# Performance work log

Hardware: AMD Instinct MI355X
Metric: run time of the kernel (lower is better)

The kernel has to match this reference:

```python
import math
import jax, jax.numpy as jnp
import numpy as np

B, N, D_FULL, M, D_V = 8, 4096, 256, 256, 256


def _phi(x, omega):
    # x: [..., N, d_full], omega: [M, d_full] -> [..., N, M]
    proj = x @ omega.T
    log_phi = proj - 0.5 * jnp.sum(x * x, axis=-1, keepdims=True)
    log_phi = log_phi - jnp.max(log_phi, axis=-1, keepdims=True)
    return jnp.exp(log_phi) / math.sqrt(omega.shape[0])


def _causal(phi_q, phi_k, V):
    # phi_q/phi_k: [B, N, M], V: [B, N, d_v]
    b, n, m = phi_q.shape
    d_v = V.shape[-1]

    def step(carry, inp):
        S, z = carry
        pq, pk, v = inp  # [B,M], [B,M], [B,d_v]
        S = S + pk[:, :, None] * v[:, None, :]          # [B, M, d_v]
        z = z + pk                                       # [B, M]
        num = jnp.einsum('bi,bij->bj', pq, S)            # [B, d_v]
        den = jnp.maximum(jnp.sum(pq * z, axis=-1), 1e-6)
        return (S, z), num / den[:, None]

    S0 = jnp.zeros((b, m, d_v), phi_q.dtype)
    z0 = jnp.zeros((b, m), phi_q.dtype)
    xs = (jnp.swapaxes(phi_q, 0, 1), jnp.swapaxes(phi_k, 0, 1), jnp.swapaxes(V, 0, 1))
    _, ys = jax.lax.scan(step, (S0, z0), xs)  # ys: [N, B, d_v]
    return jnp.swapaxes(ys, 0, 1)


def setup_inputs() -> dict:
    key = jax.random.key(0)
    kq, kk, kv, ko = jax.random.split(key, 4)
    Q = jax.random.normal(kq, (B, N, D_FULL), dtype=jnp.float32)
    K_in = jax.random.normal(kk, (B, N, D_FULL), dtype=jnp.float32)
    V = jax.random.normal(kv, (B, N, D_V), dtype=jnp.float32)
    omega = jax.random.normal(ko, (M, D_FULL), dtype=jnp.float32)
    return {"Q": Q, "K_in": K_in, "V": V, "omega": omega, "causal": 1}


def reference(Q, K_in, V, omega, causal):
    phi_q = _phi(Q, omega)
    phi_k = _phi(K_in, omega)
    if causal:
        return _causal(phi_q, phi_k, V)
    S = jnp.einsum('bni,bnj->bij', phi_k, V)          # [B, M, d_v]
    z = jnp.sum(phi_k, axis=-2)                        # [B, M]
    num = jnp.einsum('bni,bij->bnj', phi_q, S)
    den = jnp.maximum(jnp.einsum('bni,bi->bn', phi_q, z), 1e-6)
    return num / den[..., None]
```

## Files before the change

### kernel.cpp

```cpp
#include <hip/hip_runtime.h>

#define BN 8
#define NN 4096
#define DD 256
#define MM 256
#define DV 256
#define CHUNK 256
#define NC (NN / CHUNK)

using f32x4 = __attribute__((ext_vector_type(4))) float;
using s16x8 = __attribute__((ext_vector_type(8))) short;

#define MFMA16(a, b, c) __builtin_amdgcn_mfma_f32_16x16x32_bf16(a, b, c, 0, 0, 0)

__device__ __forceinline__ unsigned short f2bf(float x) {
    union { float f; unsigned int u; } v; v.f = x;
    unsigned int r = v.u + 0x7FFF + ((v.u >> 16) & 1);
    return (unsigned short)(r >> 16);
}
__device__ __forceinline__ float bf2f(unsigned short u) {
    union { unsigned int u; float f; } v; v.u = ((unsigned int)u) << 16;
    return v.f;
}

__device__ __forceinline__ void split8(const float4 xa, const float4 xb,
                                       s16x8& ah, s16x8& al)
{
    const float xs[8] = {xa.x, xa.y, xa.z, xa.w, xb.x, xb.y, xb.z, xb.w};
#pragma unroll
    for (int j = 0; j < 8; ++j) {
        union { float f; unsigned u; } v; v.f = xs[j];
        const unsigned hm = v.u & 0xFFFF0000u;
        union { unsigned u; float f; } hv; hv.u = hm;
        ah[j] = (short)(hm >> 16);
        al[j] = (short)f2bf(xs[j] - hv.f);
    }
}

__global__ __launch_bounds__(256) void omconv(
    const float* __restrict__ Om, unsigned short* __restrict__ OmH,
    unsigned short* __restrict__ OmL)
{
    const int i = blockIdx.x * 256 + threadIdx.x;
    const float4 v = *(const float4*)(Om + (size_t)i * 4);
    const float xs[4] = {v.x, v.y, v.z, v.w};
    unsigned short h[4], l[4];
#pragma unroll
    for (int j = 0; j < 4; ++j) {
        h[j] = f2bf(xs[j]);
        l[j] = f2bf(xs[j] - bf2f(h[j]));
    }
    *(uint2*)(OmH + (size_t)i * 4) = *(uint2*)h;
    *(uint2*)(OmL + (size_t)i * 4) = *(uint2*)l;
}

__global__ __launch_bounds__(256, 4) void phi_fused(
    const float* __restrict__ Qp, const float* __restrict__ Kp,
    const unsigned short* __restrict__ OmH, const unsigned short* __restrict__ OmL,
    unsigned short* __restrict__ PhiQ, unsigned short* __restrict__ PhiK,
    unsigned short* __restrict__ PhiT, float* __restrict__ Zp)
{
    const int tid = threadIdx.x;
    const int w = tid >> 6;
    const int lane = tid & 63;
    const int col = lane & 15, quad = lane >> 4;
    const bool kpath = blockIdx.x < 1024;
    const int id = kpath ? blockIdx.x : (blockIdx.x - 1024);
    const float* __restrict__ X = kpath ? Kp : Qp;
    unsigned short* __restrict__ Phi = kpath ? PhiK : PhiQ;
    const long r0 = (long)id * 32;

    __shared__ __align__(16) short AhS[32][264];
    __shared__ __align__(16) short AlS[32][264];
    __shared__ float rowmax_s[32];
    float (*red)[68] = (float(*)[68])AhS;
    unsigned short (*P)[264] = (unsigned short(*)[264])AlS;
    unsigned int* P32 = (unsigned int*)AlS;

    {
        const int rsub = lane >> 5;
        const int cc = lane & 31;
        float4 va[4], vb[4];
#pragma unroll
        for (int j = 0; j < 4; ++j) {
            const int row = w * 8 + j * 2 + rsub;
            const float* p = X + (r0 + row) * DD + cc * 8;
            va[j] = *(const float4*)p;
            vb[j] = *(const float4*)(p + 4);
        }
#pragma unroll
        for (int j = 0; j < 4; ++j) {
            const int row = w * 8 + j * 2 + rsub;
            s16x8 ah, al;
            split8(va[j], vb[j], ah, al);
            *(s16x8*)&AhS[row][cc * 8] = ah;
            *(s16x8*)&AlS[row][cc * 8] = al;
        }
    }

    f32x4 acc[2][4] = {};
    s16x8 bh0[4], bl0[4], bh1[4], bl1[4];
#pragma unroll
    for (int ct = 0; ct < 4; ++ct) {
        const size_t off = (size_t)(w * 64 + ct * 16 + col) * DD + quad * 8;
        bh0[ct] = *(const s16x8*)(OmH + off);
        bl0[ct] = *(const s16x8*)(OmL + off);
    }
    __syncthreads();

#pragma unroll
    for (int kt = 0; kt < 8; ++kt) {
        if (kt < 7) {
#pragma unroll
            for (int ct = 0; ct < 4; ++ct) {
                const size_t off = (size_t)(w * 64 + ct * 16 + col) * DD + (kt + 1) * 32 + quad * 8;
                bh1[ct] = *(const s16x8*)(OmH + off);
                bl1[ct] = *(const s16x8*)(OmL + off);
            }
        }
#pragma unroll
        for (int t = 0; t < 2; ++t) {
            const s16x8 ah = *(const s16x8*)&AhS[t * 16 + col][kt * 32 + quad * 8];
            const s16x8 al = *(const s16x8*)&AlS[t * 16 + col][kt * 32 + quad * 8];
#pragma unroll
            for (int ct = 0; ct < 4; ++ct) {
                acc[t][ct] = MFMA16(ah, bh0[ct], acc[t][ct]);
                acc[t][ct] = MFMA16(ah, bl0[ct], acc[t][ct]);
                acc[t][ct] = MFMA16(al, bh0[ct], acc[t][ct]);
            }
        }
#pragma unroll
        for (int ct = 0; ct < 4; ++ct) { bh0[ct] = bh1[ct]; bl0[ct] = bl1[ct]; }
    }

    __syncthreads();
#pragma unroll
    for (int t = 0; t < 2; ++t)
#pragma unroll
        for (int r = 0; r < 4; ++r) {
            float m = acc[t][0][r];
#pragma unroll
            for (int ct = 1; ct < 4; ++ct) m = fmaxf(m, acc[t][ct][r]);
            red[t * 16 + quad * 4 + r][w * 16 + col] = m;
        }
    __syncthreads();
    {
        const int row = tid >> 3, seg = tid & 7;
        float m = red[row][seg * 8];
#pragma unroll
        for (int j = 1; j < 8; ++j) m = fmaxf(m, red[row][seg * 8 + j]);
        m = fmaxf(m, __shfl_xor(m, 1));
        m = fmaxf(m, __shfl_xor(m, 2));
        m = fmaxf(m, __shfl_xor(m, 4));
        if (seg == 0) rowmax_s[row] = m;
    }
    __syncthreads();

#pragma unroll
    for (int t = 0; t < 2; ++t)
#pragma unroll
        for (int r = 0; r < 4; ++r) {
            const int n = t * 16 + quad * 4 + r;
            const float rm = rowmax_s[n];
#pragma unroll
            for (int ct = 0; ct < 4; ++ct) {
                const float val = __expf(acc[t][ct][r] - rm) * 0.0625f;
                const unsigned u = (unsigned)f2bf(val);
                const unsigned up = (unsigned)__shfl_xor((int)u, 1);
                if ((col & 1) == 0)
                    P32[n * 132 + w * 32 + ct * 8 + (col >> 1)] = u | (up << 16);
            }
        }
    __syncthreads();

    {
        const int t7 = tid & 7;
        const int nb = tid >> 3;
#pragma unroll
        for (int s = 0; s < 4; ++s)
            *(uint4*)(Phi + (r0 + nb) * MM + t7 * 8 + s * 64) =
                *(const uint4*)&P[nb][t7 * 8 + s * 64];
    }

    if (kpath) {
        const int b = id >> 7;
        const int c = (id >> 3) & 15;
        const int n0 = (id & 127) * 32;
        const int m0 = tid & 31;
        const int nsub = tid >> 5;
#pragma unroll
        for (int mi = 0; mi < 8; ++mi) {
            const int m = mi * 32 + m0;
            unsigned short u[4];
#pragma unroll
            for (int j = 0; j < 4; ++j) u[j] = P[nsub * 4 + j][m];
            *(uint2*)(PhiT + ((size_t)b * MM + m) * NN + n0 + nsub * 4) = *(uint2*)u;
        }
        float z = 0.f;
#pragma unroll
        for (int n = 0; n < 32; ++n) z += bf2f(P[n][tid]);
        atomicAdd(&Zp[((b * NC + c) << 8) + tid], z);
    }
}

__global__ __launch_bounds__(256) void transpose_v(
    const float* __restrict__ V, unsigned short* __restrict__ VT)
{
    const int tid = threadIdx.x;
    const int ct = blockIdx.x & 3;
    const long r0 = (long)(blockIdx.x >> 2) * 64;
    const int b = (int)(r0 >> 12);
    const int n0 = (int)(r0 & (NN - 1));
    __shared__ unsigned short T[64][72];
    const int rr = tid >> 4, cs = tid & 15;
#pragma unroll
    for (int p = 0; p < 4; ++p) {
        const int r = p * 16 + rr;
        const float4 v = *(const float4*)(V + (r0 + r) * DV + ct * 64 + cs * 4);
        T[cs * 4 + 0][r] = f2bf(v.x); T[cs * 4 + 1][r] = f2bf(v.y);
        T[cs * 4 + 2][r] = f2bf(v.z); T[cs * 4 + 3][r] = f2bf(v.w);
    }
    __syncthreads();
    const int cl = tid >> 3, ns = tid & 7;
#pragma unroll
    for (int p = 0; p < 2; ++p) {
        const int c = p * 32 + cl;
        *(uint4*)(VT + ((size_t)b * DV + ct * 64 + c) * NN + n0 + ns * 8) = *(uint4*)&T[c][ns * 8];
    }
}

__global__ __launch_bounds__(256, 3) void state_mfma(
    const unsigned short* __restrict__ VT, const unsigned short* __restrict__ PkT,
    unsigned short* __restrict__ ST)
{
    const int tid = threadIdx.x;
    const int w = tid >> 6;
    const int lane = tid & 63;
    const int col = lane & 15, quad = lane >> 4;
    const int q  = blockIdx.x >> 7;
    const int bc = blockIdx.x & 127;
    const int c  = bc & 15;
    const int b  = bc >> 4;
    const int dv0 = (q & 1) * 128 + (w & 1) * 64;
    const int m0  = (q >> 1) * 128 + (w >> 1) * 64;
    const unsigned short* Ab = VT  + (size_t)b * DV * NN + (size_t)c * CHUNK;
    const unsigned short* Bb = PkT + (size_t)b * MM * NN + (size_t)c * CHUNK;

    f32x4 acc[4][4] = {};
    s16x8 a0[4], b0[4], a1[4], b1[4];
#pragma unroll
    for (int t = 0; t < 4; ++t) {
        a0[t] = *(const s16x8*)(Ab + (size_t)(dv0 + t * 16 + col) * NN + quad * 8);
        b0[t] = *(const s16x8*)(Bb + (size_t)(m0 + t * 16 + col) * NN + quad * 8);
    }
#pragma unroll
    for (int kt = 0; kt < 8; ++kt) {
        if (kt < 7) {
#pragma unroll
            for (int t = 0; t < 4; ++t) {
                a1[t] = *(const s16x8*)(Ab + (size_t)(dv0 + t * 16 + col) * NN + (kt + 1) * 32 + quad * 8);
                b1[t] = *(const s16x8*)(Bb + (size_t)(m0 + t * 16 + col) * NN + (kt + 1) * 32 + quad * 8);
            }
        }
#pragma unroll
        for (int i = 0; i < 4; ++i)
#pragma unroll
            for (int j = 0; j < 4; ++j) acc[i][j] = MFMA16(a0[i], b0[j], acc[i][j]);
#pragma unroll
        for (int t = 0; t < 4; ++t) { a0[t] = a1[t]; b0[t] = b1[t]; }
    }
    unsigned short* Sb = ST + (((size_t)(b * NC + c)) << 16);
#pragma unroll
    for (int i = 0; i < 4; ++i)
#pragma unroll
        for (int j = 0; j < 4; ++j)
#pragma unroll
            for (int r = 0; r < 4; ++r)
                Sb[(dv0 + i * 16 + quad * 4 + r) * MM + m0 + j * 16 + col] = f2bf(acc[i][j][r]);
}

__global__ __launch_bounds__(256) void prefix2(
    unsigned short* __restrict__ ST, float* __restrict__ Z)
{
    const long idx = (long)blockIdx.x * 256 + threadIdx.x;
    const int b = (int)(idx >> 16);
    const int r = (int)(idx & 65535);
    float run = 0.f;
#pragma unroll
    for (int c = 0; c < NC; ++c) {
        const size_t off = (((size_t)(b * NC + c)) << 16) + r;
        const float v = bf2f(ST[off]);
        ST[off] = f2bf(run);
        run += v;
    }
    if (idx < BN * MM) {
        const int b2 = (int)(idx >> 8);
        const int m = (int)(idx & 255);
        float rz = 0.f;
#pragma unroll
        for (int c = 0; c < NC; ++c) {
            const size_t off = (size_t)(b2 * NC + c) * MM + m;
            const float v = Z[off];
            Z[off] = rz;
            rz += v;
        }
    }
}

__global__ __launch_bounds__(256) void out_mfma(
    const unsigned short* __restrict__ PhiQ, const unsigned short* __restrict__ PhiK,
    const unsigned short* __restrict__ VT, const unsigned short* __restrict__ ST,
    const float* __restrict__ Z, float* __restrict__ Out)
{
    const int tid = threadIdx.x;
    const int w = tid >> 6;
    const int lane = tid & 63;
    const int col = lane & 15, quad = lane >> 4;
    const int it = 3 - (blockIdx.x >> 7);
    const int low = blockIdx.x & 127;
    const int c  = low & 15;
    const int b  = low >> 4;
    const size_t chunk_row = (size_t)b * NN + (size_t)c * CHUNK;
    const unsigned short* Qrow = PhiQ + (chunk_row + it * 64) * MM;

    __shared__ unsigned short Qs[64][264];
    __shared__ unsigned short A_s[64][72];
    __shared__ float red[64][68];
    __shared__ float z_s[256];
    __shared__ float den_s[64];

    const float zval = Z[((size_t)(b * NC + c) << 8) + tid];
    s16x8 bk0[8], bk1[8];
#pragma unroll
    for (int ms = 0; ms < 8; ++ms)
        bk0[ms] = *(const s16x8*)(PhiK + (chunk_row)*MM + (size_t)(w * 16 + col) * MM + ms * 32 + quad * 8);
    uint4 qv[8];
#pragma unroll
    for (int i = 0; i < 8; ++i)
        qv[i] = *((const uint4*)Qrow + i * 256 + tid);
    z_s[tid] = zval;
#pragma unroll
    for (int i = 0; i < 8; ++i) {
        const int f = i * 256 + tid;
        *(uint4*)&Qs[f >> 5][(f & 31) * 8] = qv[i];
    }
    __syncthreads();

    f32x4 oacc[4][4] = {};
    float rsum[4][4] = {};

    for (int jt = 0; jt <= it; ++jt) {
        s16x8 bv[8];
        const unsigned short* Vbase = VT + ((size_t)b * DV + w * 64) * NN + (size_t)c * CHUNK + jt * 64;
#pragma unroll
        for (int ks2 = 0; ks2 < 2; ++ks2)
#pragma unroll
            for (int t2 = 0; t2 < 4; ++t2)
                bv[ks2 * 4 + t2] = *(const s16x8*)(Vbase + (size_t)(t2 * 16 + col) * NN + ks2 * 32 + quad * 8);
        f32x4 accA[4] = {};
#pragma unroll
        for (int ms = 0; ms < 8; ++ms)
#pragma unroll
            for (int t = 0; t < 4; ++t) {
                const s16x8 aq = *(const s16x8*)&Qs[t * 16 + col][ms * 32 + quad * 8];
                accA[t] = MFMA16(aq, bk0[ms], accA[t]);
            }
        if (jt < it) {
            const unsigned short* Krn = PhiK + (chunk_row + (jt + 1) * 64) * MM;
#pragma unroll
            for (int ms = 0; ms < 8; ++ms)
                bk1[ms] = *(const s16x8*)(Krn + (size_t)(w * 16 + col) * MM + ms * 32 + quad * 8);
        }
        __syncthreads();
#pragma unroll
        for (int t = 0; t < 4; ++t)
#pragma unroll
            for (int r = 0; r < 4; ++r) {
                const int i_loc = t * 16 + quad * 4 + r;
                const int j_loc = w * 16 + col;
                float v = (jt * 64 + j_loc <= it * 64 + i_loc) ? accA[t][r] : 0.f;
                rsum[t][r] += v;
                A_s[i_loc][j_loc] = f2bf(v);
            }
        __syncthreads();
#pragma unroll
        for (int ks2 = 0; ks2 < 2; ++ks2) {
            s16x8 av[4];
#pragma unroll
            for (int t = 0; t < 4; ++t)
                av[t] = *(const s16x8*)&A_s[t * 16 + col][ks2 * 32 + quad * 8];
#pragma unroll
            for (int t2 = 0; t2 < 4; ++t2)
#pragma unroll
                for (int t = 0; t < 4; ++t)
                    oacc[t][t2] = MFMA16(av[t], bv[ks2 * 4 + t2], oacc[t][t2]);
        }
#pragma unroll
        for (int ms = 0; ms < 8; ++ms) bk0[ms] = bk1[ms];
    }
#pragma unroll
    for (int t = 0; t < 4; ++t)
#pragma unroll
        for (int r = 0; r < 4; ++r)
            red[t * 16 + quad * 4 + r][w * 16 + col] = rsum[t][r];

    const unsigned short* Sb = ST + (((size_t)(b * NC + c)) << 16) + (size_t)(w * 64) * MM;
    s16x8 bs0[4], bs1[4];
#pragma unroll
    for (int t2 = 0; t2 < 4; ++t2)
        bs0[t2] = *(const s16x8*)(Sb + (size_t)(t2 * 16 + col) * MM + quad * 8);
#pragma unroll
    for (int ms = 0; ms < 8; ++ms) {
        if (ms < 7) {
#pragma unroll
            for (int t2 = 0; t2 < 4; ++t2)
                bs1[t2] = *(const s16x8*)(Sb + (size_t)(t2 * 16 + col) * MM + (ms + 1) * 32 + quad * 8);
        }
        s16x8 aq[4];
#pragma unroll
        for (int t = 0; t < 4; ++t)
            aq[t] = *(const s16x8*)&Qs[t * 16 + col][ms * 32 + quad * 8];
#pragma unroll
        for (int t2 = 0; t2 < 4; ++t2)
#pragma unroll
            for (int t = 0; t < 4; ++t)
                oacc[t][t2] = MFMA16(aq[t], bs0[t2], oacc[t][t2]);
#pragma unroll
        for (int t2 = 0; t2 < 4; ++t2) bs0[t2] = bs1[t2];
    }
    {
        const int i = tid & 63;
        const int seg = tid >> 6;
        float d = 0.f;
#pragma unroll
        for (int g = 0; g < 8; ++g) {
            const s16x8 qv8 = *(const s16x8*)&Qs[i][seg * 64 + g * 8];
#pragma unroll
            for (int x = 0; x < 8; ++x)
                d = fmaf(bf2f((unsigned short)qv8[x]), z_s[seg * 64 + g * 8 + x], d);
        }
        red[i][64 + seg] = d;
    }
    __syncthreads();
    if (tid < 64) {
        float s = 0.f;
#pragma unroll
        for (int j = 0; j < 68; ++j) s += red[tid][j];
        den_s[tid] = fmaxf(s, 1e-6f);
    }
    __syncthreads();
#pragma unroll
    for (int t = 0; t < 4; ++t)
#pragma unroll
        for (int r = 0; r < 4; ++r) {
            const int i_loc = t * 16 + quad * 4 + r;
            const float invd = 1.0f / den_s[i_loc];
#pragma unroll
            for (int t2 = 0; t2 < 4; ++t2)
                Out[(chunk_row + it * 64 + i_loc) * DV + w * 64 + t2 * 16 + col] = oacc[t][t2][r] * invd;
        }
}

extern "C" void kernel_launch(void* const* d_in, const int* in_sizes, int n_in,
                              void* d_out, int out_size, void* d_ws, size_t ws_size,
                              hipStream_t stream)
{
    const float* Q  = (const float*)d_in[0];
    const float* K  = (const float*)d_in[1];
    const float* V  = (const float*)d_in[2];
    const float* Om = (const float*)d_in[3];
    float* out = (float*)d_out;

    const size_t NM = (size_t)BN * NN * MM;
    unsigned short* PhiQ  = (unsigned short*)d_ws;
    unsigned short* PhiK  = PhiQ + NM;
    unsigned short* PhiKT = PhiK + NM;
    unsigned short* VT    = PhiKT + NM;
    unsigned short* ST    = VT + NM;
    unsigned short* OmH   = ST + (size_t)BN * NC * DV * MM;
    unsigned short* OmL   = OmH + (size_t)MM * DD;
    float* Z = (float*)(OmL + (size_t)MM * DD);

    hipMemsetAsync(Z, 0, (size_t)BN * NC * MM * sizeof(float), stream);
    omconv<<<dim3(64), dim3(256), 0, stream>>>(Om, OmH, OmL);
    phi_fused<<<dim3(2048), dim3(256), 0, stream>>>(Q, K, OmH, OmL, PhiQ, PhiK, PhiKT, Z);
    transpose_v<<<dim3((BN * NN) / 64 * 4), dim3(256), 0, stream>>>(V, VT);
    state_mfma<<<dim3(BN * NC * 4), dim3(256), 0, stream>>>(VT, PhiKT, ST);
    prefix2<<<dim3((BN * DV * MM) / 256), dim3(256), 0, stream>>>(ST, Z);
    out_mfma<<<dim3(BN * NC * 4), dim3(256), 0, stream>>>(PhiQ, PhiK, VT, ST, Z, out);
}
```

Measured before the change: 266.8 us.

## Pre-swizzle omega into MFMA fragment layout and widen phi load/store patterns

The omega conversion kernel now writes the hi/lo bf16 halves in a per-wave, per-k-tile, per-lane fragment order, so phi_fused loads its B operands as fully contiguous 16-byte-per-lane reads instead of strided row reads. The X tile load now uses one float4 per lane per row (fully coalesced 1 KB rows) rather than two float4s per lane. The PhiT transpose store now writes 16-byte chunks covering 8 tokens instead of 8-byte chunks. This reduces uncoalesced global traffic in the phi stage, at the cost of a layout coupling between omconv and phi_fused, plus possible LDS bank conflicts from the narrower 8-byte shared stores.

```diff
diff --git a/kernel.cpp b/kernel.cpp
--- a/kernel.cpp
+++ b/kernel.cpp
@@ -23,17 +23,16 @@
     return v.f;
 }
 
-__device__ __forceinline__ void split8(const float4 xa, const float4 xb,
-                                       s16x8& ah, s16x8& al)
-{
-    const float xs[8] = {xa.x, xa.y, xa.z, xa.w, xb.x, xb.y, xb.z, xb.w};
-#pragma unroll
-    for (int j = 0; j < 8; ++j) {
+__device__ __forceinline__ void split4(const float4 x, unsigned short h[4], unsigned short l[4])
+{
+    const float xs[4] = {x.x, x.y, x.z, x.w};
+#pragma unroll
+    for (int j = 0; j < 4; ++j) {
         union { float f; unsigned u; } v; v.f = xs[j];
         const unsigned hm = v.u & 0xFFFF0000u;
         union { unsigned u; float f; } hv; hv.u = hm;
-        ah[j] = (short)(hm >> 16);
-        al[j] = (short)f2bf(xs[j] - hv.f);
+        h[j] = (unsigned short)(hm >> 16);
+        l[j] = f2bf(xs[j] - hv.f);
     }
 }
 
@@ -42,16 +41,17 @@
     unsigned short* __restrict__ OmL)
 {
     const int i = blockIdx.x * 256 + threadIdx.x;
-    const float4 v = *(const float4*)(Om + (size_t)i * 4);
-    const float xs[4] = {v.x, v.y, v.z, v.w};
+    const int row = i >> 6;
+    const int k0  = (i & 63) * 4;
+    const float4 v = *(const float4*)(Om + (size_t)row * DD + k0);
+    const int wv = row >> 6, ct = (row >> 4) & 3, colL = row & 15;
+    const int kt = k0 >> 5, quad = (k0 >> 3) & 3, e0 = k0 & 7;
+    const int lanep = quad * 16 + colL;
+    const size_t off = ((size_t)((wv * 8 + kt) * 4 + ct) * 64 + lanep) * 8 + e0;
     unsigned short h[4], l[4];
-#pragma unroll
-    for (int j = 0; j < 4; ++j) {
-        h[j] = f2bf(xs[j]);
-        l[j] = f2bf(xs[j] - bf2f(h[j]));
-    }
-    *(uint2*)(OmH + (size_t)i * 4) = *(uint2*)h;
-    *(uint2*)(OmL + (size_t)i * 4) = *(uint2*)l;
+    split4(v, h, l);
+    *(uint2*)(OmH + off) = *(uint2*)h;
+    *(uint2*)(OmL + off) = *(uint2*)l;
 }
 
 __global__ __launch_bounds__(256, 4) void phi_fused(
@@ -78,33 +78,31 @@
     unsigned int* P32 = (unsigned int*)AlS;
 
     {
-        const int rsub = lane >> 5;
-        const int cc = lane & 31;
-        float4 va[4], vb[4];
-#pragma unroll
-        for (int j = 0; j < 4; ++j) {
-            const int row = w * 8 + j * 2 + rsub;
-            const float* p = X + (r0 + row) * DD + cc * 8;
-            va[j] = *(const float4*)p;
-            vb[j] = *(const float4*)(p + 4);
-        }
-#pragma unroll
-        for (int j = 0; j < 4; ++j) {
-            const int row = w * 8 + j * 2 + rsub;
-            s16x8 ah, al;
-            split8(va[j], vb[j], ah, al);
-            *(s16x8*)&AhS[row][cc * 8] = ah;
-            *(s16x8*)&AlS[row][cc * 8] = al;
-        }
-    }
-
+        float4 xv[8];
+#pragma unroll
+        for (int j = 0; j < 8; ++j) {
+            const int row = w * 8 + j;
+            xv[j] = *(const float4*)(X + (r0 + row) * DD + lane * 4);
+        }
+#pragma unroll
+        for (int j = 0; j < 8; ++j) {
+            const int row = w * 8 + j;
+            unsigned short h[4], l[4];
+            split4(xv[j], h, l);
+            *(uint2*)&AhS[row][lane * 4] = *(uint2*)h;
+            *(uint2*)&AlS[row][lane * 4] = *(uint2*)l;
+        }
+    }
+
+    const unsigned short* OmHw = OmH + (size_t)w * 8 * 4 * 512;
+    const unsigned short* OmLw = OmL + (size_t)w * 8 * 4 * 512;
     f32x4 acc[2][4] = {};
     s16x8 bh0[4], bl0[4], bh1[4], bl1[4];
 #pragma unroll
     for (int ct = 0; ct < 4; ++ct) {
-        const size_t off = (size_t)(w * 64 + ct * 16 + col) * DD + quad * 8;
-        bh0[ct] = *(const s16x8*)(OmH + off);
-        bl0[ct] = *(const s16x8*)(OmL + off);
+        const size_t off = ((size_t)ct * 64 + lane) * 8;
+        bh0[ct] = *(const s16x8*)(OmHw + off);
+        bl0[ct] = *(const s16x8*)(OmLw + off);
     }
     __syncthreads();
 
@@ -113,9 +111,9 @@
         if (kt < 7) {
 #pragma unroll
             for (int ct = 0; ct < 4; ++ct) {
-                const size_t off = (size_t)(w * 64 + ct * 16 + col) * DD + (kt + 1) * 32 + quad * 8;
-                bh1[ct] = *(const s16x8*)(OmH + off);
-                bl1[ct] = *(const s16x8*)(OmL + off);
+                const size_t off = ((size_t)((kt + 1) * 4 + ct) * 64 + lane) * 8;
+                bh1[ct] = *(const s16x8*)(OmHw + off);
+                bl1[ct] = *(const s16x8*)(OmLw + off);
             }
         }
 #pragma unroll
@@ -186,15 +184,15 @@
         const int b = id >> 7;
         const int c = (id >> 3) & 15;
         const int n0 = (id & 127) * 32;
-        const int m0 = tid & 31;
-        const int nsub = tid >> 5;
-#pragma unroll
-        for (int mi = 0; mi < 8; ++mi) {
-            const int m = mi * 32 + m0;
-            unsigned short u[4];
-#pragma unroll
-            for (int j = 0; j < 4; ++j) u[j] = P[nsub * 4 + j][m];
-            *(uint2*)(PhiT + ((size_t)b * MM + m) * NN + n0 + nsub * 4) = *(uint2*)u;
+        const int nb4 = (tid & 3) * 8;
+        const int mBase = tid >> 2;
+#pragma unroll
+        for (int mi = 0; mi < 4; ++mi) {
+            const int m = mi * 64 + mBase;
+            unsigned short u[8];
+#pragma unroll
+            for (int j = 0; j < 8; ++j) u[j] = P[nb4 + j][m];
+            *(uint4*)(PhiT + ((size_t)b * MM + m) * NN + n0 + nb4) = *(uint4*)u;
         }
         float z = 0.f;
 #pragma unroll
```

Measured after the change: 230.7 us. 13.5% less time.
